# Performance work log

Hardware: AMD Instinct MI355X
Metric: run time of the kernel (lower is better)

Reference implementation:

```python
import jax, jax.numpy as jnp
import numpy as np

N_EMBD = 1024
HEAD_SIZE = 128
BLOCK_SIZE = 2048
B, T = 8, 2048

def setup_inputs() -> dict:
    key = jax.random.key(0)
    kx, kq, kk, kv = jax.random.split(key, 4)
    x = jax.random.normal(kx, (B, T, N_EMBD), dtype=jnp.float32)
    # nn.Linear(n_embd, head_size, bias=False) weights: [head_size, n_embd]
    s = 1.0 / np.sqrt(N_EMBD)
    Wq = jax.random.uniform(kq, (HEAD_SIZE, N_EMBD), jnp.float32, -s, s)
    Wk = jax.random.uniform(kk, (HEAD_SIZE, N_EMBD), jnp.float32, -s, s)
    Wv = jax.random.uniform(kv, (HEAD_SIZE, N_EMBD), jnp.float32, -s, s)
    return {"x": x, "Wq": Wq, "Wk": Wk, "Wv": Wv}

def reference(x, Wq, Wk, Wv):
    # q,k,v: [B,T,H]
    q = jnp.einsum('btc,hc->bth', x, Wq)
    k = jnp.einsum('btc,hc->bth', x, Wk)
    v = jnp.einsum('btc,hc->bth', x, Wv)
    scale = k.shape[-1] ** -0.5
    wei = jnp.einsum('bth,bsh->bts', q, k) * scale  # [B,T,T]
    Tq = q.shape[1]
    causal = jnp.tril(jnp.ones((Tq, Tq), dtype=bool))
    wei = jnp.where(causal[None, :, :], wei, -jnp.inf)
    wei = jax.nn.softmax(wei, axis=-1)
    out = jnp.einsum('bts,bsh->bth', wei, v)  # [B,T,H]
    return out
```

## Files before the change

### kernel.cpp

```cpp
#include <hip/hip_runtime.h>

#define B_ 8
#define T_ 2048
#define C_ 1024
#define H_ 128
#define BT_ (B_ * T_)

typedef __attribute__((ext_vector_type(8))) short short8;
typedef __attribute__((ext_vector_type(4))) float f32x4;
typedef __attribute__((ext_vector_type(16))) float f32x16;
typedef unsigned short u16;

#define SSCALE 0.12753257708482632f

static __device__ __forceinline__ u16 f2bf(float f) {
    union { float f; unsigned u; } x; x.f = f;
    unsigned r = x.u + 0x7fffu + ((x.u >> 16) & 1u);
    return (u16)(r >> 16);
}

static __device__ __forceinline__ unsigned long long pack4bf(float a, float b, float c, float d) {
    return (unsigned long long)f2bf(a) |
           ((unsigned long long)f2bf(b) << 16) |
           ((unsigned long long)f2bf(c) << 32) |
           ((unsigned long long)f2bf(d) << 48);
}

static __device__ __forceinline__ unsigned cvtpk(float lo, float hi) {
    unsigned r;
    asm("v_cvt_pk_bf16_f32 %0, %1, %2" : "=v"(r) : "v"(lo), "v"(hi));
    return r;
}

static __device__ __forceinline__ void pl32swap(unsigned &a, unsigned &b) {
    asm volatile("v_permlane32_swap_b32 %0, %1" : "+v"(a), "+v"(b));
}
static __device__ __forceinline__ void pl32swapf(float &a, float &b) {
    asm volatile("v_permlane32_swap_b32 %0, %1" : "+v"(a), "+v"(b));
}

#define GLDS16(g, l)                                                            \
    __builtin_amdgcn_global_load_lds(                                           \
        (const __attribute__((address_space(1))) void*)(g),                     \
        (__attribute__((address_space(3))) void*)(l), 16, 0, 0)

__global__ __launch_bounds__(256) void wconv_kernel(
    const float* __restrict__ Wq, const float* __restrict__ Wk,
    const float* __restrict__ Wv, u16* __restrict__ wb)
{
    int t = blockIdx.x * 256 + threadIdx.x;
    int e = t * 8;
    const float* __restrict__ src = (e < 131072) ? Wq : (e < 262144 ? Wk : Wv);
    const float sc = (e < 131072) ? SSCALE : 1.0f;
    int off = e & 131071;
    float4 f0 = *(const float4*)&src[off];
    float4 f1 = *(const float4*)&src[off + 4];
    union { unsigned long long u[2]; uint4 v; } pk;
    pk.u[0] = pack4bf(f0.x * sc, f0.y * sc, f0.z * sc, f0.w * sc);
    pk.u[1] = pack4bf(f1.x * sc, f1.y * sc, f1.z * sc, f1.w * sc);
    *(uint4*)&wb[e] = pk.v;
}

__global__ __launch_bounds__(512) void proj_kernel(
    const float* __restrict__ x, const u16* __restrict__ wb,
    u16* __restrict__ qo, u16* __restrict__ ko, u16* __restrict__ vt)
{
    __shared__ union {
        struct { u16 a[2][64 * 64]; u16 w[2][384 * 64]; } s;
        u16 c[64 * 136];
    } lds;

    const int tid = threadIdx.x;
    const int lane = tid & 63;
    const int wid = tid >> 6;
    const int wr = wid >> 2;
    const int wc = wid & 3;
    const int m0 = blockIdx.x * 64;

    const int gr = lane >> 3, gc = lane & 7;

    float4 va0[2], va1[2], va2[2];

    f32x4 acc[2][6];
    #pragma unroll
    for (int i = 0; i < 2; i++)
        #pragma unroll
        for (int j = 0; j < 6; j++) acc[i][j] = f32x4{0.f, 0.f, 0.f, 0.f};

#define ALOAD(slot, kt)                                                          \
    {                                                                            \
        _Pragma("unroll")                                                        \
        for (int p = 0; p < 2; p++) {                                            \
            int idx = p * 512 + tid, r = idx >> 4, cc = (idx & 15) * 4;          \
            slot[p] = *(const float4*)&x[(size_t)(m0 + r) * C_ + (kt) * 64 + cc];\
        }                                                                        \
    }
#define AWRITE(slot, buf)                                                        \
    {                                                                            \
        _Pragma("unroll")                                                        \
        for (int p = 0; p < 2; p++) {                                            \
            int idx = p * 512 + tid, r = idx >> 4, cc = (idx & 15) * 4;          \
            int byte = (r * 128 + cc * 2) ^ ((r & 7) << 4);                      \
            *(unsigned long long*)((char*)lds.s.a[buf] + byte) =                 \
                pack4bf(slot[p].x, slot[p].y, slot[p].z, slot[p].w);             \
        }                                                                        \
    }
#define WISSUE(kt, buf)                                                          \
    {                                                                            \
        _Pragma("unroll")                                                        \
        for (int jj = 0; jj < 6; jj++) {                                         \
            int j = wid * 6 + jj;                                                \
            int row = j * 8 + gr;                                                \
            GLDS16(wb + (size_t)row * C_ + (kt) * 64 + ((gc ^ gr) * 8),          \
                   (char*)lds.s.w[buf] + j * 1024);                              \
        }                                                                        \
    }

    ALOAD(va0, 0)
    AWRITE(va0, 0)
    WISSUE(0, 0)
    __builtin_amdgcn_sched_barrier(0);
    ALOAD(va1, 1)
    ALOAD(va2, 2)
    asm volatile("s_waitcnt vmcnt(4) lgkmcnt(0)" ::: "memory");
    __builtin_amdgcn_s_barrier();

    #pragma unroll
    for (int k = 0; k < 16; k++) {
        const int pb = k & 1;
        if (k + 1 <= 15) WISSUE(k + 1, pb ^ 1)
        __builtin_amdgcn_sched_barrier(0);
        if (k + 3 <= 15) {
            if ((k % 3) == 0) ALOAD(va0, k + 3)
            else if ((k % 3) == 1) ALOAD(va1, k + 3)
            else ALOAD(va2, k + 3)
        }

        #pragma unroll
        for (int ks = 0; ks < 2; ks++) {
            short8 af[2], bf[6];
            #pragma unroll
            for (int i = 0; i < 2; i++) {
                int row = wr * 32 + i * 16 + (lane & 15);
                int byte = (row * 128 + ks * 64 + (lane >> 4) * 16) ^ ((row & 7) << 4);
                af[i] = *(const short8*)((const char*)lds.s.a[pb] + byte);
            }
            #pragma unroll
            for (int j = 0; j < 6; j++) {
                int n = wc * 96 + j * 16 + (lane & 15);
                int byte = (n * 128 + ks * 64 + (lane >> 4) * 16) ^ ((n & 7) << 4);
                bf[j] = *(const short8*)((const char*)lds.s.w[pb] + byte);
            }
            #pragma unroll
            for (int i = 0; i < 2; i++)
                #pragma unroll
                for (int j = 0; j < 6; j++)
                    acc[i][j] = __builtin_amdgcn_mfma_f32_16x16x32_bf16(
                        af[i], bf[j], acc[i][j], 0, 0, 0);
        }

        if (k + 1 <= 15) {
            if (((k + 1) % 3) == 0) AWRITE(va0, pb ^ 1)
            else if (((k + 1) % 3) == 1) AWRITE(va1, pb ^ 1)
            else AWRITE(va2, pb ^ 1)
        }

        if (k <= 12)      asm volatile("s_waitcnt vmcnt(2) lgkmcnt(0)" ::: "memory");
        else              asm volatile("s_waitcnt vmcnt(0) lgkmcnt(0)" ::: "memory");
        __builtin_amdgcn_s_barrier();
    }
#undef ALOAD
#undef AWRITE
#undef WISSUE

    const int b = m0 / T_;
    const int tloc = m0 % T_;
    #pragma unroll
    for (int i = 0; i < 2; i++) {
        #pragma unroll
        for (int j = 0; j < 6; j++) {
            int n = wc * 96 + j * 16 + (lane & 15);
            int wdx = n >> 7;
            int rowb = wr * 32 + i * 16 + (lane >> 4) * 4;
            if (wdx < 2) {
                u16* __restrict__ dst = wdx ? ko : qo;
                int col = n & 127;
                #pragma unroll
                for (int r = 0; r < 4; r++)
                    dst[(size_t)(m0 + rowb + r) * H_ + col] = f2bf(acc[i][j][r]);
            } else {
                int h = n - 256;
                #pragma unroll
                for (int r = 0; r < 4; r++)
                    lds.c[(rowb + r) * 136 + h] = f2bf(acc[i][j][r]);
            }
        }
    }
    __syncthreads();
    #pragma unroll
    for (int p = 0; p < 2; p++) {
        int idx = p * 512 + tid;
        int h = idx >> 3, tg = idx & 7;
        u16 pk[8];
        #pragma unroll
        for (int jj = 0; jj < 8; jj++) pk[jj] = lds.c[(tg * 8 + jj) * 136 + h];
        *(short8*)&vt[((size_t)b * H_ + h) * T_ + tloc + tg * 8] = *(const short8*)pk;
    }
}

template<int S>
__global__ __launch_bounds__(256, 2) void attn32_kernel(
    const u16* __restrict__ q, const u16* __restrict__ k, const u16* __restrict__ vt,
    float* __restrict__ out, float* __restrict__ po, float* __restrict__ lp)
{
    __shared__ u16 kt[2][64 * 128];
    __shared__ u16 vtt[2][128 * 64];

    const int tid = threadIdx.x, lane = tid & 63, wid = tid >> 6;
    const int hi = lane >> 5, l31 = lane & 31;

    const int bid = blockIdx.x;
    int b, qt, p;
    if (S == 1)      { b = bid >> 4; qt = bid & 15; p = 0; }
    else if (S == 2) { b = bid >> 5; qt = bid & 15; p = (bid >> 4) & 1; }
    else             { b = bid >> 6; qt = bid & 15; p = (bid >> 4) & 3; }
    const int total = 2 * qt + 2;
    const int s0 = p * total / S, s1 = (p + 1) * total / S;
    const int qbase = qt * 128;
    const int qrow = qbase + wid * 32 + l31;

    short8 qf[8];
    #pragma unroll
    for (int ks = 0; ks < 8; ks++)
        qf[ks] = *(const short8*)&q[((size_t)b * T_ + qrow) * H_ + ks * 16 + hi * 8];

    f32x16 ot0, ot1, ot2, ot3;
    #pragma unroll
    for (int i = 0; i < 16; i++) { ot0[i] = 0.f; ot1[i] = 0.f; ot2[i] = 0.f; ot3[i] = 0.f; }
    float lsum = 0.f;

    const u16* __restrict__ kb = k + (size_t)b * T_ * H_;
    const u16* __restrict__ vb = vt + (size_t)b * H_ * T_;

    auto stage = [&](int s, int pbuf) {
        const int kvbase = s * 64;
        #pragma unroll
        for (int jj = 0; jj < 4; jj++) {
            int j = wid * 4 + jj;
            int r = j * 4 + (lane >> 4), c = lane & 15;
            GLDS16(kb + (size_t)(kvbase + r) * H_ + ((c ^ (r & 7)) * 8),
                   (char*)kt[pbuf] + j * 1024);
        }
        #pragma unroll
        for (int jj = 0; jj < 4; jj++) {
            int j = wid * 4 + jj;
            int h = j * 8 + (lane >> 3), c = lane & 7;
            GLDS16(vb + (size_t)h * T_ + kvbase + ((c ^ (h & 7)) * 8),
                   (char*)vtt[pbuf] + j * 1024);
        }
    };

    if (s0 < s1) {
        stage(s0, 0);
        asm volatile("s_waitcnt vmcnt(0)" ::: "memory");
        __builtin_amdgcn_s_barrier();
    }

    for (int s = s0; s < s1; s++) {
        const int pb = (s - s0) & 1;
        if (s + 1 < s1) stage(s + 1, pb ^ 1);
        const int kvbase = s * 64;
        const char* __restrict__ ktb = (const char*)kt[pb];
        const char* __restrict__ vtb = (const char*)vtt[pb];

        f32x16 sa0, sa1;
        #pragma unroll
        for (int i = 0; i < 16; i++) { sa0[i] = 0.f; sa1[i] = 0.f; }
        __builtin_amdgcn_s_setprio(1);
        #pragma unroll
        for (int ks = 0; ks < 8; ks++) {
            const int ch = ks * 2 + hi;
            const int r0 = l31, r1 = 32 + l31;
            short8 a0 = *(const short8*)(ktb + r0 * 256 + ((ch ^ (r0 & 7)) << 4));
            short8 a1 = *(const short8*)(ktb + r1 * 256 + ((ch ^ (r1 & 7)) << 4));
            sa0 = __builtin_amdgcn_mfma_f32_32x32x16_bf16(a0, qf[ks], sa0, 0, 0, 0);
            sa1 = __builtin_amdgcn_mfma_f32_32x32x16_bf16(a1, qf[ks], sa1, 0, 0, 0);
        }
        __builtin_amdgcn_s_setprio(0);

        const bool dm = (s >= 2 * qt);
        #pragma unroll
        for (int r = 0; r < 16; r++) {
            const int crow = (r & 3) + 8 * (r >> 2) + 4 * hi;
            float e0 = exp2f(sa0[r]);
            float e1 = exp2f(sa1[r]);
            if (dm) {
                if (kvbase + crow > qrow) e0 = 0.f;
                if (kvbase + 32 + crow > qrow) e1 = 0.f;
            }
            sa0[r] = e0; sa1[r] = e1;
            lsum += e0 + e1;
        }

        unsigned u0[8], u1[8];
        #pragma unroll
        for (int j = 0; j < 8; j++) {
            u0[j] = cvtpk(sa0[2 * j], sa0[2 * j + 1]);
            u1[j] = cvtpk(sa1[2 * j], sa1[2 * j + 1]);
        }
        pl32swap(u0[0], u0[2]); pl32swap(u0[1], u0[3]);
        pl32swap(u0[4], u0[6]); pl32swap(u0[5], u0[7]);
        pl32swap(u1[0], u1[2]); pl32swap(u1[1], u1[3]);
        pl32swap(u1[4], u1[6]); pl32swap(u1[5], u1[7]);
        union PKU { unsigned w[4]; short8 v; };
        PKU f0, f1, f2, f3;
        f0.w[0] = u0[0]; f0.w[1] = u0[1]; f0.w[2] = u0[2]; f0.w[3] = u0[3];
        f1.w[0] = u0[4]; f1.w[1] = u0[5]; f1.w[2] = u0[6]; f1.w[3] = u0[7];
        f2.w[0] = u1[0]; f2.w[1] = u1[1]; f2.w[2] = u1[2]; f2.w[3] = u1[3];
        f3.w[0] = u1[4]; f3.w[1] = u1[5]; f3.w[2] = u1[6]; f3.w[3] = u1[7];

        __builtin_amdgcn_s_setprio(1);
#define PV_DT(OT, DT)                                                               \
        {                                                                           \
            const int d = DT * 32 + l31;                                            \
            const char* vrow = vtb + d * 128;                                       \
            const int sw = d & 7;                                                   \
            short8 va0 = *(const short8*)(vrow + (((0 + hi) ^ sw) << 4));           \
            short8 va1 = *(const short8*)(vrow + (((2 + hi) ^ sw) << 4));           \
            short8 va2 = *(const short8*)(vrow + (((4 + hi) ^ sw) << 4));           \
            short8 va3 = *(const short8*)(vrow + (((6 + hi) ^ sw) << 4));           \
            OT = __builtin_amdgcn_mfma_f32_32x32x16_bf16(va0, f0.v, OT, 0, 0, 0);   \
            OT = __builtin_amdgcn_mfma_f32_32x32x16_bf16(va1, f1.v, OT, 0, 0, 0);   \
            OT = __builtin_amdgcn_mfma_f32_32x32x16_bf16(va2, f2.v, OT, 0, 0, 0);   \
            OT = __builtin_amdgcn_mfma_f32_32x32x16_bf16(va3, f3.v, OT, 0, 0, 0);   \
        }
        PV_DT(ot0, 0) PV_DT(ot1, 1) PV_DT(ot2, 2) PV_DT(ot3, 3)
#undef PV_DT
        __builtin_amdgcn_s_setprio(0);

        asm volatile("s_waitcnt vmcnt(0)" ::: "memory");
        __builtin_amdgcn_s_barrier();
    }

    float la = lsum, lb = lsum;
    pl32swapf(la, lb);
    const float ltot = la + lb;

    float* __restrict__ dst = (S == 1 || p == 0) ? out : (po + (size_t)(p - 1) * BT_ * H_);
    const float rinv = (S == 1) ? (1.0f / ltot) : 1.0f;
    float* __restrict__ orow = &dst[((size_t)b * T_ + qrow) * H_];
#define WR_DT(OT, DT)                                                   \
    {                                                                   \
        _Pragma("unroll")                                               \
        for (int g = 0; g < 4; g++) {                                   \
            float4 w4;                                                  \
            w4.x = OT[4 * g + 0] * rinv; w4.y = OT[4 * g + 1] * rinv;   \
            w4.z = OT[4 * g + 2] * rinv; w4.w = OT[4 * g + 3] * rinv;   \
            *(float4*)&orow[DT * 32 + g * 8 + hi * 4] = w4;             \
        }                                                               \
    }
    WR_DT(ot0, 0) WR_DT(ot1, 1) WR_DT(ot2, 2) WR_DT(ot3, 3)
#undef WR_DT
    if (S > 1 && lane < 32)
        lp[(size_t)p * BT_ + b * T_ + qrow] = ltot;
}

template<int S>
__global__ __launch_bounds__(256) void combineS_kernel(
    float* __restrict__ out, const float* __restrict__ po, const float* __restrict__ lp)
{
    int i = blockIdx.x * 256 + threadIdx.x;
    int row = i >> 5;
    float lt = lp[row];
    #pragma unroll
    for (int pp = 1; pp < S; pp++) lt += lp[(size_t)pp * BT_ + row];
    float inv = 1.0f / lt;
    float4 a = ((const float4*)out)[i];
    #pragma unroll
    for (int pp = 1; pp < S; pp++) {
        float4 c = ((const float4*)(po + (size_t)(pp - 1) * BT_ * H_))[i];
        a.x += c.x; a.y += c.y; a.z += c.z; a.w += c.w;
    }
    a.x *= inv; a.y *= inv; a.z *= inv; a.w *= inv;
    ((float4*)out)[i] = a;
}

extern "C" void kernel_launch(void* const* d_in, const int* in_sizes, int n_in,
                              void* d_out, int out_size, void* d_ws, size_t ws_size,
                              hipStream_t stream) {
    const float* x  = (const float*)d_in[0];
    const float* Wq = (const float*)d_in[1];
    const float* Wk = (const float*)d_in[2];
    const float* Wv = (const float*)d_in[3];

    u16* q  = (u16*)d_ws;
    u16* kk = q + (size_t)BT_ * H_;
    u16* vt = kk + (size_t)BT_ * H_;
    u16* wb = vt + (size_t)BT_ * H_;
    const size_t po_off = (size_t)3 * BT_ * H_ * 2 + 393216 * 2;
    float* po = (float*)((char*)d_ws + po_off);
    const size_t obytes = (size_t)BT_ * H_ * 4;
    const size_t need4 = po_off + 3 * obytes + (size_t)4 * BT_ * 4;
    const size_t need2 = po_off + 1 * obytes + (size_t)2 * BT_ * 4;

    wconv_kernel<<<192, 256, 0, stream>>>(Wq, Wk, Wv, wb);
    proj_kernel<<<256, 512, 0, stream>>>(x, wb, q, kk, vt);

    if (ws_size >= need4) {
        float* lpx = (float*)((char*)d_ws + po_off + 3 * obytes);
        attn32_kernel<4><<<512, 256, 0, stream>>>(q, kk, vt, (float*)d_out, po, lpx);
        combineS_kernel<4><<<2048, 256, 0, stream>>>((float*)d_out, po, lpx);
    } else if (ws_size >= need2) {
        float* lpx = (float*)((char*)d_ws + po_off + 1 * obytes);
        attn32_kernel<2><<<256, 256, 0, stream>>>(q, kk, vt, (float*)d_out, po, lpx);
        combineS_kernel<2><<<2048, 256, 0, stream>>>((float*)d_out, po, lpx);
    } else {
        attn32_kernel<1><<<128, 256, 0, stream>>>(q, kk, vt, (float*)d_out, nullptr, nullptr);
    }
}
```

Baseline: 154.1 us.

## Store split-KV partials in bf16, reverse q-tile order, split row-sum accumulators

```diff
diff --git a/kernel.cpp b/kernel.cpp
--- a/kernel.cpp
+++ b/kernel.cpp
@@ -17,6 +17,11 @@
     union { float f; unsigned u; } x; x.f = f;
     unsigned r = x.u + 0x7fffu + ((x.u >> 16) & 1u);
     return (u16)(r >> 16);
+}
+
+static __device__ __forceinline__ float bf2f(u16 v) {
+    union { unsigned u; float f; } x; x.u = ((unsigned)v) << 16;
+    return x.f;
 }
 
 static __device__ __forceinline__ unsigned long long pack4bf(float a, float b, float c, float d) {
@@ -211,7 +216,7 @@
 template<int S>
 __global__ __launch_bounds__(256, 2) void attn32_kernel(
     const u16* __restrict__ q, const u16* __restrict__ k, const u16* __restrict__ vt,
-    float* __restrict__ out, float* __restrict__ po, float* __restrict__ lp)
+    float* __restrict__ out, u16* __restrict__ po, float* __restrict__ lp)
 {
     __shared__ u16 kt[2][64 * 128];
     __shared__ u16 vtt[2][128 * 64];
@@ -221,9 +226,9 @@
 
     const int bid = blockIdx.x;
     int b, qt, p;
-    if (S == 1)      { b = bid >> 4; qt = bid & 15; p = 0; }
-    else if (S == 2) { b = bid >> 5; qt = bid & 15; p = (bid >> 4) & 1; }
-    else             { b = bid >> 6; qt = bid & 15; p = (bid >> 4) & 3; }
+    if (S == 1)      { b = bid >> 4; qt = 15 - (bid & 15); p = 0; }
+    else if (S == 2) { b = bid >> 5; qt = 15 - (bid & 15); p = (bid >> 4) & 1; }
+    else             { b = bid >> 6; qt = 15 - (bid & 15); p = (bid >> 4) & 3; }
     const int total = 2 * qt + 2;
     const int s0 = p * total / S, s1 = (p + 1) * total / S;
     const int qbase = qt * 128;
@@ -237,7 +242,7 @@
     f32x16 ot0, ot1, ot2, ot3;
     #pragma unroll
     for (int i = 0; i < 16; i++) { ot0[i] = 0.f; ot1[i] = 0.f; ot2[i] = 0.f; ot3[i] = 0.f; }
-    float lsum = 0.f;
+    float ls0 = 0.f, ls1 = 0.f, ls2 = 0.f, ls3 = 0.f;
 
     const u16* __restrict__ kb = k + (size_t)b * T_ * H_;
     const u16* __restrict__ vb = vt + (size_t)b * H_ * T_;
@@ -299,7 +304,10 @@
                 if (kvbase + 32 + crow > qrow) e1 = 0.f;
             }
             sa0[r] = e0; sa1[r] = e1;
-            lsum += e0 + e1;
+            if ((r & 3) == 0)      { ls0 += e0; ls1 += e1; }
+            else if ((r & 3) == 1) { ls1 += e0; ls2 += e1; }
+            else if ((r & 3) == 2) { ls2 += e0; ls3 += e1; }
+            else                   { ls3 += e0; ls0 += e1; }
         }
 
         unsigned u0[8], u1[8];
@@ -342,47 +350,66 @@
         __builtin_amdgcn_s_barrier();
     }
 
+    float lsum = (ls0 + ls1) + (ls2 + ls3);
     float la = lsum, lb = lsum;
     pl32swapf(la, lb);
     const float ltot = la + lb;
 
-    float* __restrict__ dst = (S == 1 || p == 0) ? out : (po + (size_t)(p - 1) * BT_ * H_);
-    const float rinv = (S == 1) ? (1.0f / ltot) : 1.0f;
-    float* __restrict__ orow = &dst[((size_t)b * T_ + qrow) * H_];
+    if (S == 1) {
+        const float rinv = 1.0f / ltot;
+        float* __restrict__ orow = &out[((size_t)b * T_ + qrow) * H_];
 #define WR_DT(OT, DT)                                                   \
-    {                                                                   \
-        _Pragma("unroll")                                               \
-        for (int g = 0; g < 4; g++) {                                   \
-            float4 w4;                                                  \
-            w4.x = OT[4 * g + 0] * rinv; w4.y = OT[4 * g + 1] * rinv;   \
-            w4.z = OT[4 * g + 2] * rinv; w4.w = OT[4 * g + 3] * rinv;   \
-            *(float4*)&orow[DT * 32 + g * 8 + hi * 4] = w4;             \
-        }                                                               \
-    }
-    WR_DT(ot0, 0) WR_DT(ot1, 1) WR_DT(ot2, 2) WR_DT(ot3, 3)
+        {                                                               \
+            _Pragma("unroll")                                           \
+            for (int g = 0; g < 4; g++) {                               \
+                float4 w4;                                              \
+                w4.x = OT[4 * g + 0] * rinv; w4.y = OT[4 * g + 1] * rinv;\
+                w4.z = OT[4 * g + 2] * rinv; w4.w = OT[4 * g + 3] * rinv;\
+                *(float4*)&orow[DT * 32 + g * 8 + hi * 4] = w4;         \
+            }                                                           \
+        }
+        WR_DT(ot0, 0) WR_DT(ot1, 1) WR_DT(ot2, 2) WR_DT(ot3, 3)
 #undef WR_DT
-    if (S > 1 && lane < 32)
-        lp[(size_t)p * BT_ + b * T_ + qrow] = ltot;
+    } else {
+        u16* __restrict__ prow = &po[((size_t)p * BT_ + (size_t)b * T_ + qrow) * H_];
+#define WP_DT(OT, DT)                                                   \
+        {                                                               \
+            _Pragma("unroll")                                           \
+            for (int g = 0; g < 4; g++) {                               \
+                *(unsigned long long*)&prow[DT * 32 + g * 8 + hi * 4] = \
+                    pack4bf(OT[4 * g + 0], OT[4 * g + 1],               \
+                            OT[4 * g + 2], OT[4 * g + 3]);              \
+            }                                                           \
+        }
+        WP_DT(ot0, 0) WP_DT(ot1, 1) WP_DT(ot2, 2) WP_DT(ot3, 3)
+#undef WP_DT
+        if (lane < 32)
+            lp[(size_t)p * BT_ + b * T_ + qrow] = ltot;
+    }
 }
 
 template<int S>
 __global__ __launch_bounds__(256) void combineS_kernel(
-    float* __restrict__ out, const float* __restrict__ po, const float* __restrict__ lp)
+    float* __restrict__ out, const u16* __restrict__ po, const float* __restrict__ lp)
 {
     int i = blockIdx.x * 256 + threadIdx.x;
-    int row = i >> 5;
+    int row = i >> 4;
     float lt = lp[row];
     #pragma unroll
     for (int pp = 1; pp < S; pp++) lt += lp[(size_t)pp * BT_ + row];
     float inv = 1.0f / lt;
-    float4 a = ((const float4*)out)[i];
-    #pragma unroll
-    for (int pp = 1; pp < S; pp++) {
-        float4 c = ((const float4*)(po + (size_t)(pp - 1) * BT_ * H_))[i];
-        a.x += c.x; a.y += c.y; a.z += c.z; a.w += c.w;
-    }
-    a.x *= inv; a.y *= inv; a.z *= inv; a.w *= inv;
-    ((float4*)out)[i] = a;
+    float a[8] = {0.f, 0.f, 0.f, 0.f, 0.f, 0.f, 0.f, 0.f};
+    #pragma unroll
+    for (int pp = 0; pp < S; pp++) {
+        short8 v = *(const short8*)&po[(size_t)pp * BT_ * H_ + (size_t)i * 8];
+        #pragma unroll
+        for (int j = 0; j < 8; j++) a[j] += bf2f((u16)v[j]);
+    }
+    float4 w0, w1;
+    w0.x = a[0] * inv; w0.y = a[1] * inv; w0.z = a[2] * inv; w0.w = a[3] * inv;
+    w1.x = a[4] * inv; w1.y = a[5] * inv; w1.z = a[6] * inv; w1.w = a[7] * inv;
+    *(float4*)&out[(size_t)i * 8]     = w0;
+    *(float4*)&out[(size_t)i * 8 + 4] = w1;
 }
 
 extern "C" void kernel_launch(void* const* d_in, const int* in_sizes, int n_in,
@@ -398,22 +425,22 @@
     u16* vt = kk + (size_t)BT_ * H_;
     u16* wb = vt + (size_t)BT_ * H_;
     const size_t po_off = (size_t)3 * BT_ * H_ * 2 + 393216 * 2;
-    float* po = (float*)((char*)d_ws + po_off);
-    const size_t obytes = (size_t)BT_ * H_ * 4;
-    const size_t need4 = po_off + 3 * obytes + (size_t)4 * BT_ * 4;
-    const size_t need2 = po_off + 1 * obytes + (size_t)2 * BT_ * 4;
+    u16* po = (u16*)((char*)d_ws + po_off);
+    const size_t pbytes = (size_t)BT_ * H_ * 2;
+    const size_t need4 = po_off + 4 * pbytes + (size_t)4 * BT_ * 4;
+    const size_t need2 = po_off + 2 * pbytes + (size_t)2 * BT_ * 4;
 
     wconv_kernel<<<192, 256, 0, stream>>>(Wq, Wk, Wv, wb);
     proj_kernel<<<256, 512, 0, stream>>>(x, wb, q, kk, vt);
 
     if (ws_size >= need4) {
-        float* lpx = (float*)((char*)d_ws + po_off + 3 * obytes);
+        float* lpx = (float*)((char*)d_ws + po_off + 4 * pbytes);
         attn32_kernel<4><<<512, 256, 0, stream>>>(q, kk, vt, (float*)d_out, po, lpx);
-        combineS_kernel<4><<<2048, 256, 0, stream>>>((float*)d_out, po, lpx);
+        combineS_kernel<4><<<1024, 256, 0, stream>>>((float*)d_out, po, lpx);
     } else if (ws_size >= need2) {
-        float* lpx = (float*)((char*)d_ws + po_off + 1 * obytes);
+        float* lpx = (float*)((char*)d_ws + po_off + 2 * pbytes);
         attn32_kernel<2><<<256, 256, 0, stream>>>(q, kk, vt, (float*)d_out, po, lpx);
-        combineS_kernel<2><<<2048, 256, 0, stream>>>((float*)d_out, po, lpx);
+        combineS_kernel<2><<<1024, 256, 0, stream>>>((float*)d_out, po, lpx);
     } else {
         attn32_kernel<1><<<128, 256, 0, stream>>>(q, kk, vt, (float*)d_out, nullptr, nullptr);
     }
```

After: 153.3 us. No clear change (-0.5%).
